# Kernel tuning notes

Hardware: AMD Instinct MI355X
Metric: run time of the kernel (lower is better)

Reference implementation:

```python
import jax, jax.numpy as jnp
import numpy as np

# ---------- helpers ----------

def _sqdist(a, b):
    # a: (B,n,3), b: (B,m,3) -> squared distances (B,n,m)
    return (jnp.sum(a * a, -1)[..., :, None] + jnp.sum(b * b, -1)[..., None, :]
            - 2.0 * jnp.einsum('bnd,bmd->bnm', a, b))

_gather = jax.vmap(lambda pts, idx: pts[idx])  # (N,C),(S,K)->(S,K,C) over batch


def _fps(xyz, npoint):
    # farthest point sampling; indices are non-differentiable (as in CUDA op)
    xyz = jax.lax.stop_gradient(xyz)
    B, N, _ = xyz.shape
    mind0 = jnp.sum((xyz - xyz[:, :1]) ** 2, -1)  # dist to point 0

    def step(mind, _):
        idx = jnp.argmax(mind, -1)                       # (B,)
        nxt = jnp.take_along_axis(xyz, idx[:, None, None], 1)  # (B,1,3)
        mind = jnp.minimum(mind, jnp.sum((xyz - nxt) ** 2, -1))
        return mind, idx.astype(jnp.int32)

    _, idxs = jax.lax.scan(step, mind0, None, length=npoint - 1)
    return jnp.concatenate([jnp.zeros((B, 1), jnp.int32), idxs.T], 1)  # (B,npoint)


def _ball_query(xyz, new_xyz, radius, nsample):
    # first nsample points within radius of each center, pad with first hit
    d2 = jax.lax.stop_gradient(_sqdist(new_xyz, xyz))  # (B,S,N)
    N = xyz.shape[1]
    mask = d2 < radius * radius
    key = jnp.where(mask, 0, N) + jnp.arange(N, dtype=jnp.int32)  # in-ball first, original order
    order = jnp.argsort(key, -1)
    idx = order[..., :nsample]
    cnt = mask.sum(-1, keepdims=True)
    return jnp.where(jnp.arange(nsample) < cnt, idx, idx[..., :1])


def _mlp(x, params):
    # shared MLP: 1x1 conv (+BN folded: default eval stats -> affine bias) + ReLU
    for W, b in params:
        x = jax.nn.relu(jnp.einsum('...c,co->...o', x, W) + b)
    return x


def _sa(xyz, feats, npoint, radius, nsample, params):
    # PointnetSAModuleVotes: FPS + ball-query + group(use_xyz, normalize_xyz) + MLP + max-pool
    inds = _fps(xyz, npoint)
    new_xyz = _gather(xyz, inds)                              # (B,S,3)
    idx = _ball_query(xyz, new_xyz, radius, nsample)          # (B,S,K)
    g = (_gather(xyz, idx) - new_xyz[:, :, None, :]) / radius  # normalize_xyz
    if feats is not None:
        g = jnp.concatenate([g, _gather(feats, idx)], -1)     # use_xyz: xyz first
    g = _mlp(g, params)
    return new_xyz, jnp.max(g, 2), inds                       # max over nsample


def _fp(unknown, known, feats1, feats2, params):
    # PointnetFPModule: 3-NN inverse-(squared)distance interpolation + MLP
    d2 = jax.lax.stop_gradient(_sqdist(unknown, known))       # (B,n,m)
    negd, idx = jax.lax.top_k(-d2, 3)
    d = jnp.maximum(-negd, 0.0)
    w = 1.0 / (d + 1e-8)
    w = w / jnp.sum(w, -1, keepdims=True)                     # (B,n,3)
    interp = jnp.sum(w[..., None] * _gather(feats2, idx), 2)  # (B,n,C2)
    return _mlp(jnp.concatenate([feats1, interp], -1), params)


_SPECS = {
    'sa1': [(3, 32), (32, 32), (32, 64)],
    'sa2': [(67, 64), (64, 128)],
    'sa3': [(131, 128), (128, 256)],
    'sa4': [(259, 256), (256, 256)],
    'fp1': [(512, 256), (256, 128)],
    'fp2': [(256, 128), (128, 64)],
}


def setup_inputs() -> dict:
    key = jax.random.key(0)
    ks = iter(jax.random.split(key, 64))
    inp = {'pointcloud': jax.random.uniform(next(ks), (4, 32768, 3), jnp.float32)}
    for name, dims in _SPECS.items():
        for i, (ci, co) in enumerate(dims):
            inp[f'{name}_w{i}'] = jax.random.normal(next(ks), (ci, co), jnp.float32) * 0.02
            inp[f'{name}_b{i}'] = jnp.zeros((co,), jnp.float32)
    return inp


def reference(pointcloud,
              sa1_w0, sa1_b0, sa1_w1, sa1_b1, sa1_w2, sa1_b2,
              sa2_w0, sa2_b0, sa2_w1, sa2_b1,
              sa3_w0, sa3_b0, sa3_w1, sa3_b1,
              sa4_w0, sa4_b0, sa4_w1, sa4_b1,
              fp1_w0, fp1_b0, fp1_w1, fp1_b1,
              fp2_w0, fp2_b0, fp2_w1, fp2_b1):
    P = {
        'sa1': [(sa1_w0, sa1_b0), (sa1_w1, sa1_b1), (sa1_w2, sa1_b2)],
        'sa2': [(sa2_w0, sa2_b0), (sa2_w1, sa2_b1)],
        'sa3': [(sa3_w0, sa3_b0), (sa3_w1, sa3_b1)],
        'sa4': [(sa4_w0, sa4_b0), (sa4_w1, sa4_b1)],
        'fp1': [(fp1_w0, fp1_b0), (fp1_w1, fp1_b1)],
        'fp2': [(fp2_w0, fp2_b0), (fp2_w1, fp2_b1)],
    }
    xyz = pointcloud[..., :3]  # input_feature_dim = 0 -> no extra features
    xyz1, f1, _ = _sa(xyz, None, 512, 0.1, 64, P['sa1'])
    xyz2, f2, _ = _sa(xyz1, f1, 256, 0.2, 32, P['sa2'])
    xyz3, f3, _ = _sa(xyz2, f2, 64, 0.4, 16, P['sa3'])
    xyz4, f4, _ = _sa(xyz3, f3, 16, 0.8, 16, P['sa4'])
    f = _fp(xyz3, xyz4, f3, f4, P['fp1'])   # (B,64,128)
    f = _fp(xyz2, xyz3, f2, f, P['fp2'])    # (B,256,64) == torch feats.transpose(1,2)
    return f, xyz2
```

## Files before the change

### kernel.cpp

```cpp
#include <hip/hip_runtime.h>
#include <cstddef>


__device__ __forceinline__ float sqd(float x, float y, float z, float qx, float qy, float qz) {
#pragma clang fp contract(off)
    float dx = x - qx, dy = y - qy, dz = z - qz;
    return (dx * dx + dy * dy) + dz * dz;
}

__device__ __forceinline__ float sum3sq(float x, float y, float z) {
#pragma clang fp contract(off)
    return (x * x + y * y) + z * z;
}

__device__ __forceinline__ float sqd_dot(float ax, float ay, float az, float sa_,
                                         float bx, float by, float bz) {
#pragma clang fp contract(off)
    float sb = (bx * bx + by * by) + bz * bz;
    float dt = (ax * bx + ay * by) + az * bz;
    return (sa_ + sb) - 2.0f * dt;
}

__device__ __forceinline__ unsigned long long packkey(float v, int orig) {
    return ((unsigned long long)__float_as_uint(v) << 32) | (unsigned)(~orig);
}


__global__ __launch_bounds__(512) void fps_sub(const float* __restrict__ xyz,
                                               int* __restrict__ inds,
                                               float4* __restrict__ SPall,
                                               float* __restrict__ gout) {
    const int b = blockIdx.x, t = threadIdx.x, w = t >> 6, l = t & 63;
    const float* __restrict__ P = xyz + (size_t)b * 32768 * 3;
    float4* __restrict__ SP = SPall + (size_t)b * 32768;

    __shared__ float mind[32768];
    __shared__ int   cntS[512], offS[512], curS[512];
    __shared__ unsigned long long bkeyS[512];
    __shared__ float bxS[512], byS[512], bzS[512];
    __shared__ unsigned long long candK[8];
    __shared__ int   candB[8];
    __shared__ float bbS[6];
    __shared__ float scr[48];
    __shared__ int   qcntS;

    float mnx = 1e30f, mny = 1e30f, mnz = 1e30f;
    float mxx = -1e30f, mxy = -1e30f, mxz = -1e30f;
    for (int p = t; p < 32768; p += 512) {
        const float x = P[3 * p], y = P[3 * p + 1], z = P[3 * p + 2];
        mnx = fminf(mnx, x); mxx = fmaxf(mxx, x);
        mny = fminf(mny, y); mxy = fmaxf(mxy, y);
        mnz = fminf(mnz, z); mxz = fmaxf(mxz, z);
    }
#pragma unroll
    for (int o = 1; o < 64; o <<= 1) {
        mnx = fminf(mnx, __shfl_xor(mnx, o)); mxx = fmaxf(mxx, __shfl_xor(mxx, o));
        mny = fminf(mny, __shfl_xor(mny, o)); mxy = fmaxf(mxy, __shfl_xor(mxy, o));
        mnz = fminf(mnz, __shfl_xor(mnz, o)); mxz = fmaxf(mxz, __shfl_xor(mxz, o));
    }
    if (l == 0) {
        scr[w] = mnx; scr[8 + w] = mny; scr[16 + w] = mnz;
        scr[24 + w] = mxx; scr[32 + w] = mxy; scr[40 + w] = mxz;
    }
    __syncthreads();
    if (t == 0) {
        float a0 = 1e30f, a1 = 1e30f, a2 = 1e30f, a3 = -1e30f, a4 = -1e30f, a5 = -1e30f;
        for (int i = 0; i < 8; ++i) {
            a0 = fminf(a0, scr[i]);      a1 = fminf(a1, scr[8 + i]);
            a2 = fminf(a2, scr[16 + i]); a3 = fmaxf(a3, scr[24 + i]);
            a4 = fmaxf(a4, scr[32 + i]); a5 = fmaxf(a5, scr[40 + i]);
        }
        bbS[0] = a0; bbS[1] = a1; bbS[2] = a2; bbS[3] = a3; bbS[4] = a4; bbS[5] = a5;
        qcntS = 0;
    }
    __syncthreads();
    const float bx0 = bbS[0], by0 = bbS[1], bz0 = bbS[2];
    const float ex = bbS[3] - bx0, ey = bbS[4] - by0, ez = bbS[5] - bz0;
    const float ivx = ex > 1e-20f ? 8.0f / ex : 0.0f;
    const float ivy = ey > 1e-20f ? 8.0f / ey : 0.0f;
    const float ivz = ez > 1e-20f ? 8.0f / ez : 0.0f;

    cntS[t] = 0;
    __syncthreads();
    for (int p = t; p < 32768; p += 512) {
        const float x = P[3 * p], y = P[3 * p + 1], z = P[3 * p + 2];
        const int ix = min(7, (int)((x - bx0) * ivx));
        const int iy = min(7, (int)((y - by0) * ivy));
        const int iz = min(7, (int)((z - bz0) * ivz));
        atomicAdd(&cntS[(iz * 8 + iy) * 8 + ix], 1);
    }
    __syncthreads();

    offS[t] = cntS[t];
    __syncthreads();
    for (int d = 1; d < 512; d <<= 1) {
        const int v = (t >= d) ? offS[t - d] : 0;
        __syncthreads();
        offS[t] += v;
        __syncthreads();
    }
    const int myexc = offS[t] - cntS[t];
    offS[t] = myexc;
    curS[t] = myexc;
    __syncthreads();

    for (int p = t; p < 32768; p += 512) {
        const float x = P[3 * p], y = P[3 * p + 1], z = P[3 * p + 2];
        const int ix = min(7, (int)((x - bx0) * ivx));
        const int iy = min(7, (int)((y - by0) * ivy));
        const int iz = min(7, (int)((z - bz0) * ivz));
        const int pos = atomicAdd(&curS[(iz * 8 + iy) * 8 + ix], 1);
        SP[pos] = make_float4(x, y, z, __int_as_float(p));
    }
    for (int s = t; s < 32768; s += 512) mind[s] = 1e30f;
    const int myCnt = cntS[t];
    bkeyS[t] = (myCnt > 0) ? packkey(1e30f, 0x7fffffff) : 0ull;
    bxS[t] = 0.f; byS[t] = 0.f; bzS[t] = 0.f;
    if (t == 0) {
        inds[b * 512] = 0;
        gout[(size_t)b * 512 * 3 + 0] = P[0];
        gout[(size_t)b * 512 * 3 + 1] = P[1];
        gout[(size_t)b * 512 * 3 + 2] = P[2];
    }

    const int oix = t & 7, oiy = (t >> 3) & 7, oiz = t >> 6;
    const float gwx = ex * 0.125f, gwy = ey * 0.125f, gwz = ez * 0.125f;
    const float x0o = bx0 + oix * gwx, x1o = x0o + gwx;
    const float y0o = by0 + oiy * gwy, y1o = y0o + gwy;
    const float z0o = bz0 + oiz * gwz, z1o = z0o + gwz;

    const int g  = l >> 4;
    const int lg = l & 15;
    const int sg = w * 4 + g;

    float qx = P[0], qy = P[1], qz = P[2];
    __syncthreads();

    for (int k = 1; k < 512; ++k) {
        const float ddx = fmaxf(fmaxf(x0o - qx, qx - x1o), 0.0f);
        const float ddy = fmaxf(fmaxf(y0o - qy, qy - y1o), 0.0f);
        const float ddz = fmaxf(fmaxf(z0o - qz, qz - z1o), 0.0f);
        const float d2m = (ddx * ddx + ddy * ddy) + ddz * ddz;
        const float bm = __uint_as_float((unsigned)(bkeyS[t] >> 32));
        const bool act = (myCnt > 0) && (d2m <= bm * 1.0001f + 1e-9f);
        const unsigned long long pmask = __ballot(act);
        const int wcnt = __popcll(pmask);
        int wbase = 0;
        if (l == 0 && wcnt) wbase = atomicAdd(&qcntS, wcnt);
        wbase = __shfl(wbase, 0);
        if (act) curS[wbase + __popcll(pmask & ((1ull << l) - 1ull))] = t;
        __syncthreads();
        const int A = qcntS;

        for (int e = sg; e < A; e += 32) {
            const int bu = curS[e];
            const int base = offS[bu], cnt = cntS[bu];
            unsigned long long key = 0ull;
            int klane = l;
            float cx = 0.f, cy = 0.f, cz = 0.f;
            for (int c = lg; c < cnt; c += 16) {
                const float4 pt = SP[base + c];
                const float m = mind[base + c];
                const float d2 = sqd(pt.x, pt.y, pt.z, qx, qy, qz);
                const float nm = fminf(m, d2);
                mind[base + c] = nm;
                const unsigned long long kk = packkey(nm, __float_as_int(pt.w));
                if (kk > key) { key = kk; cx = pt.x; cy = pt.y; cz = pt.z; }
            }
#pragma unroll
            for (int s = 1; s < 16; s <<= 1) {
                const unsigned long long ok = __shfl_xor(key, s);
                const int ol2 = __shfl_xor(klane, s);
                if (ok > key) { key = ok; klane = ol2; }
            }
            const float wx = __shfl(cx, klane), wy = __shfl(cy, klane), wz = __shfl(cz, klane);
            if (lg == 0) {
                bkeyS[bu] = key;
                bxS[bu] = wx; byS[bu] = wy; bzS[bu] = wz;
            }
        }
        __syncthreads();

        unsigned long long key = bkeyS[t];
        int bu2 = t;
#pragma unroll
        for (int s = 1; s < 64; s <<= 1) {
            const unsigned long long ok = __shfl_xor(key, s);
            const int ob = __shfl_xor(bu2, s);
            if (ok > key) { key = ok; bu2 = ob; }
        }
        if (l == 0) { candK[w] = key; candB[w] = bu2; }
        if (t == 0) qcntS = 0;
        __syncthreads();
        unsigned long long wk = candK[0]; int wb = candB[0];
#pragma unroll
        for (int j = 1; j < 8; ++j) {
            const unsigned long long k2 = candK[j];
            if (k2 > wk) { wk = k2; wb = candB[j]; }
        }
        qx = bxS[wb]; qy = byS[wb]; qz = bzS[wb];
        if (t == 0) {
            inds[b * 512 + k] = (int)~(unsigned)wk;
            gout[((size_t)b * 512 + k) * 3 + 0] = qx;
            gout[((size_t)b * 512 + k) * 3 + 1] = qy;
            gout[((size_t)b * 512 + k) * 3 + 2] = qz;
        }
    }
}


template <int N, int NPOINT>
__global__ __launch_bounds__(64) void fps_small(const float* __restrict__ pts,
                                                float* __restrict__ gout) {
    constexpr int PPT = N / 64;
    const int b = blockIdx.x, l = threadIdx.x;
    const float* __restrict__ P = pts + (size_t)b * N * 3;
    float px[PPT], py[PPT], pz[PPT], md[PPT];
#pragma unroll
    for (int j = 0; j < PPT; ++j) {
        const int p = l + 64 * j;
        px[j] = P[p * 3]; py[j] = P[p * 3 + 1]; pz[j] = P[p * 3 + 2];
        md[j] = 1e30f;
    }
    float qx = P[0], qy = P[1], qz = P[2];
    if (l == 0) {
        gout[(size_t)b * NPOINT * 3 + 0] = qx;
        gout[(size_t)b * NPOINT * 3 + 1] = qy;
        gout[(size_t)b * NPOINT * 3 + 2] = qz;
    }
    for (int k = 1; k < NPOINT; ++k) {
        float bv = -1.0f;
        int   bi = 0;
#pragma unroll
        for (int j = 0; j < PPT; ++j) {
            md[j] = fminf(md[j], sqd(px[j], py[j], pz[j], qx, qy, qz));
            if (md[j] > bv) { bv = md[j]; bi = l + 64 * j; }
        }
#pragma unroll
        for (int off = 1; off < 64; off <<= 1) {
            float ov = __shfl_xor(bv, off);
            int   oi = __shfl_xor(bi, off);
            if (ov > bv || (ov == bv && oi < bi)) { bv = ov; bi = oi; }
        }
        const int ol = bi & 63, js = bi >> 6;
        float sx = px[0], sy = py[0], sz = pz[0];
#pragma unroll
        for (int j = 1; j < PPT; ++j) {
            if (j == js) { sx = px[j]; sy = py[j]; sz = pz[j]; }
        }
        qx = __shfl(sx, ol); qy = __shfl(sy, ol); qz = __shfl(sz, ol);
        if (l == 0) {
            gout[((size_t)b * NPOINT + k) * 3 + 0] = qx;
            gout[((size_t)b * NPOINT + k) * 3 + 1] = qy;
            gout[((size_t)b * NPOINT + k) * 3 + 2] = qz;
        }
    }
}


__global__ __launch_bounds__(64) void sa1_fused(
    const float* __restrict__ xyz, const float* __restrict__ centers,
    const float* __restrict__ w0, const float* __restrict__ b0,
    const float* __restrict__ w1, const float* __restrict__ b1,
    const float* __restrict__ w2, const float* __restrict__ b2,
    float* __restrict__ outf, float r2, float r) {
    const int gc = blockIdx.x;
    const int b  = gc >> 9;
    const int l  = threadIdx.x;
    const float* __restrict__ P = xyz + (size_t)b * 32768 * 3;
    const float* cp = centers + (size_t)gc * 3;
    const float cx = cp[0], cy = cp[1], cz = cp[2];
    const float sa_ = sum3sq(cx, cy, cz);
    __shared__ int idxS[64];

    int cnt = 0, first = -1;
    float nx = P[l * 3], ny = P[l * 3 + 1], nz = P[l * 3 + 2];
    for (int i0 = 0; i0 < 32768; i0 += 64) {
        const float bx = nx, by = ny, bz = nz;
        if (i0 + 64 < 32768) {
            const int ip = (i0 + 64 + l) * 3;
            nx = P[ip]; ny = P[ip + 1]; nz = P[ip + 2];
        }
        const float d2 = sqd_dot(cx, cy, cz, sa_, bx, by, bz);
        const bool in = d2 < r2;
        const unsigned long long mask = __ballot(in);
        if (first < 0 && mask != 0ull) first = i0 + __builtin_ctzll(mask);
        const int pos = cnt + __popcll(mask & ((1ull << l) - 1ull));
        if (in && pos < 64) idxS[pos] = i0 + l;
        cnt += __popcll(mask);
        if (cnt >= 64) break;
    }
    if (first < 0) first = 0;
    for (int p2 = cnt + l; p2 < 64; p2 += 64) idxS[p2] = first;
    __syncthreads();

    const int n = idxS[l];
    const float* pp = P + (size_t)n * 3;
    float gi[3];
    gi[0] = (pp[0] - cx) / r; gi[1] = (pp[1] - cy) / r; gi[2] = (pp[2] - cz) / r;
    float h1[32];
#pragma unroll
    for (int o = 0; o < 32; ++o) {
        float acc = b0[o];
#pragma unroll
        for (int k = 0; k < 3; ++k) acc += gi[k] * w0[k * 32 + o];
        h1[o] = fmaxf(acc, 0.f);
    }
    float h2[32];
#pragma unroll
    for (int o = 0; o < 32; ++o) {
        float acc = b1[o];
#pragma unroll
        for (int k = 0; k < 32; ++k) acc += h1[k] * w1[k * 32 + o];
        h2[o] = fmaxf(acc, 0.f);
    }
    __shared__ float hs[64][65];
#pragma unroll
    for (int o = 0; o < 64; ++o) {
        float acc = b2[o];
#pragma unroll
        for (int k = 0; k < 32; ++k) acc += h2[k] * w2[k * 64 + o];
        hs[l][o] = fmaxf(acc, 0.f);
    }
    __syncthreads();
    float mx = hs[0][l];
    for (int s2 = 1; s2 < 64; ++s2) mx = fmaxf(mx, hs[s2][l]);
    outf[(size_t)gc * 64 + l] = mx;
}


template <int NS>
__global__ __launch_bounds__(256) void bqb(const float* __restrict__ xyz_src,
                                           const float* __restrict__ centers,
                                           const float* __restrict__ feats,
                                           float* __restrict__ g,
                                           int N, int M, int CF, float r, float r2) {
    const int wv = blockIdx.x * 4 + (threadIdx.x >> 6);
    const int w  = threadIdx.x >> 6;
    const int l  = threadIdx.x & 63;
    const int b  = wv / M;
    __shared__ int idxS[4][NS];
    const float* cp = centers + (size_t)wv * 3;
    const float ax = cp[0], ay = cp[1], az = cp[2];
    const float sa_ = sum3sq(ax, ay, az);
    const float* __restrict__ P = xyz_src + (size_t)b * N * 3;

    int cnt = 0, first = -1;
    float nx = P[l * 3], ny = P[l * 3 + 1], nz = P[l * 3 + 2];
    for (int i0 = 0; i0 < N; i0 += 64) {
        const float bx = nx, by = ny, bz = nz;
        if (i0 + 64 < N) {
            const int ip = (i0 + 64 + l) * 3;
            nx = P[ip]; ny = P[ip + 1]; nz = P[ip + 2];
        }
        const float d2 = sqd_dot(ax, ay, az, sa_, bx, by, bz);
        const bool in = d2 < r2;
        const unsigned long long mask = __ballot(in);
        if (first < 0 && mask != 0ull) first = i0 + __builtin_ctzll(mask);
        const int pos = cnt + __popcll(mask & ((1ull << l) - 1ull));
        if (in && pos < NS) idxS[w][pos] = i0 + l;
        cnt += __popcll(mask);
        if (cnt >= NS) break;
    }
    if (first < 0) first = 0;
    for (int p2 = cnt + l; p2 < NS; p2 += 64) idxS[w][p2] = first;
    __syncthreads();

    for (int s = 0; s < NS; ++s) {
        const int n = idxS[w][s];
        float* go = g + ((size_t)wv * NS + s) * (3 + CF);
        const float* pp = P + (size_t)n * 3;
        if (l < 3) go[l] = (pp[l] - cp[l]) / r;
        for (int c = l; c < CF; c += 64) go[3 + c] = feats[((size_t)b * N + n) * CF + c];
    }
}


__global__ void dense_relu(const float* __restrict__ X, const float* __restrict__ Wm,
                           const float* __restrict__ bias, float* __restrict__ Y,
                           int M, int CI, int CO) {
    const int co = blockIdx.x * 64 + threadIdx.x;
    const int m  = blockIdx.y * 4 + threadIdx.y;
    const float* x = X + (size_t)m * CI;
    float acc = bias[co];
#pragma unroll 4
    for (int k = 0; k < CI; ++k) acc += x[k] * Wm[(size_t)k * CO + co];
    Y[(size_t)m * CO + co] = fmaxf(acc, 0.f);
}


__global__ void dense_relu_max(const float* __restrict__ X, const float* __restrict__ Wm,
                               const float* __restrict__ bias, float* __restrict__ F,
                               int NS, int CI, int CO) {
    const int co = blockIdx.x * 64 + threadIdx.x;
    const int bm = blockIdx.y;
    const float b0 = bias[co];
    float mx = -1e30f;
    for (int s = 0; s < NS; ++s) {
        const float* x = X + ((size_t)bm * NS + s) * CI;
        float acc = b0;
#pragma unroll 4
        for (int k = 0; k < CI; ++k) acc += x[k] * Wm[(size_t)k * CO + co];
        mx = fmaxf(mx, fmaxf(acc, 0.f));
    }
    F[(size_t)bm * CO + co] = mx;
}


__global__ void fp_nn(const float* __restrict__ unk, const float* __restrict__ kn,
                      int* __restrict__ nni, float* __restrict__ nnw, int NU, int NK) {
    const int t = blockIdx.x * blockDim.x + threadIdx.x;
    const int b = t / NU;
    const float* u = unk + (size_t)t * 3;
    const float ax = u[0], ay = u[1], az = u[2];
    const float sa_ = sum3sq(ax, ay, az);
    const float* K = kn + (size_t)b * NK * 3;
    float v0 = 1e30f, v1 = 1e30f, v2 = 1e30f;
    int   j0 = 0, j1 = 0, j2 = 0;
    for (int k = 0; k < NK; ++k) {
        const float d2 = sqd_dot(ax, ay, az, sa_, K[k * 3], K[k * 3 + 1], K[k * 3 + 2]);
        if (d2 < v0)      { v2 = v1; j2 = j1; v1 = v0; j1 = j0; v0 = d2; j0 = k; }
        else if (d2 < v1) { v2 = v1; j2 = j1; v1 = d2; j1 = k; }
        else if (d2 < v2) { v2 = d2; j2 = k; }
    }
    const float d0 = fmaxf(v0, 0.f), d1 = fmaxf(v1, 0.f), dd2 = fmaxf(v2, 0.f);
    float w0 = 1.f / (d0 + 1e-8f), w1 = 1.f / (d1 + 1e-8f), w2 = 1.f / (dd2 + 1e-8f);
    const float s = (w0 + w1) + w2;
    nnw[t * 3] = w0 / s; nnw[t * 3 + 1] = w1 / s; nnw[t * 3 + 2] = w2 / s;
    nni[t * 3] = j0; nni[t * 3 + 1] = j1; nni[t * 3 + 2] = j2;
}


__global__ void dense_fp(const float* __restrict__ f1c, const float* __restrict__ f2c,
                         const int* __restrict__ nni, const float* __restrict__ nnw,
                         const float* __restrict__ Wm, const float* __restrict__ bias,
                         float* __restrict__ Y, int NU, int NK, int C1c, int C2c, int CO) {
    const int co = blockIdx.x * 64 + threadIdx.x;
    const int m  = blockIdx.y * 4 + threadIdx.y;
    const int b  = m / NU;
    const int i0 = nni[m * 3], i1 = nni[m * 3 + 1], i2 = nni[m * 3 + 2];
    const float w0 = nnw[m * 3], w1 = nnw[m * 3 + 1], w2 = nnw[m * 3 + 2];
    const float* x1 = f1c + (size_t)m * C1c;
    const float* a  = f2c + ((size_t)b * NK + i0) * C2c;
    const float* bb = f2c + ((size_t)b * NK + i1) * C2c;
    const float* cc = f2c + ((size_t)b * NK + i2) * C2c;
    float acc = bias[co];
#pragma unroll 4
    for (int k = 0; k < C1c; ++k) acc += x1[k] * Wm[(size_t)k * CO + co];
#pragma unroll 4
    for (int k = 0; k < C2c; ++k) {
        const float xi = (w0 * a[k] + w1 * bb[k]) + w2 * cc[k];
        acc += xi * Wm[(size_t)(C1c + k) * CO + co];
    }
    Y[(size_t)m * CO + co] = fmaxf(acc, 0.f);
}

__global__ void copyf(const float* __restrict__ src, float* __restrict__ dst, int n) {
    const int i = blockIdx.x * 256 + threadIdx.x;
    if (i < n) dst[i] = src[i];
}


extern "C" void kernel_launch(void* const* d_in, const int* in_sizes, int n_in,
                              void* d_out, int out_size, void* d_ws, size_t ws_size,
                              hipStream_t stream) {
    const float* xyz  = (const float*)d_in[0];
    const float* s1w0 = (const float*)d_in[1],  *s1b0 = (const float*)d_in[2];
    const float* s1w1 = (const float*)d_in[3],  *s1b1 = (const float*)d_in[4];
    const float* s1w2 = (const float*)d_in[5],  *s1b2 = (const float*)d_in[6];
    const float* s2w0 = (const float*)d_in[7],  *s2b0 = (const float*)d_in[8];
    const float* s2w1 = (const float*)d_in[9],  *s2b1 = (const float*)d_in[10];
    const float* s3w0 = (const float*)d_in[11], *s3b0 = (const float*)d_in[12];
    const float* s3w1 = (const float*)d_in[13], *s3b1 = (const float*)d_in[14];
    const float* s4w0 = (const float*)d_in[15], *s4b0 = (const float*)d_in[16];
    const float* s4w1 = (const float*)d_in[17], *s4b1 = (const float*)d_in[18];
    const float* p1w0 = (const float*)d_in[19], *p1b0 = (const float*)d_in[20];
    const float* p1w1 = (const float*)d_in[21], *p1b1 = (const float*)d_in[22];
    const float* p2w0 = (const float*)d_in[23], *p2b0 = (const float*)d_in[24];
    const float* p2w1 = (const float*)d_in[25], *p2b1 = (const float*)d_in[26];
    float* out = (float*)d_out;
    float* W = (float*)d_ws;

    size_t off = 0;
    auto A_ = [&](size_t n) { size_t o = off; off += (n + 63) & ~(size_t)63; return o; };
    const size_t o_inds1 = A_(4 * 512);
    const size_t o_xyz1  = A_(4 * 512 * 3);
    const size_t o_f1    = A_(4 * 512 * 64);
    const size_t o_xyz2  = A_(4 * 256 * 3);
    const size_t o_f2    = A_(4 * 256 * 128);
    const size_t o_xyz3  = A_(4 * 64 * 3);
    const size_t o_f3    = A_(4 * 64 * 256);
    const size_t o_xyz4  = A_(4 * 16 * 3);
    const size_t o_f4    = A_(4 * 16 * 256);
    const size_t o_f5    = A_(4 * 64 * 128);
    const size_t o_nni1  = A_(4 * 64 * 3);
    const size_t o_nnw1  = A_(4 * 64 * 3);
    const size_t o_nni2  = A_(4 * 256 * 3);
    const size_t o_nnw2  = A_(4 * 256 * 3);
    const size_t o_sort  = A_((size_t)4 * 32768 * 4);
    const size_t o_bufA  = A_((size_t)32768 * 128);
    const size_t o_bufB  = A_((size_t)32768 * 64);
    if (off * sizeof(float) > ws_size) return;

    int*   inds1 = (int*)(W + o_inds1); float* xyz1 = W + o_xyz1;
    float* f1    = W + o_f1;
    float* xyz2  = W + o_xyz2;          float* f2   = W + o_f2;
    float* xyz3  = W + o_xyz3;          float* f3   = W + o_f3;
    float* xyz4  = W + o_xyz4;          float* f4   = W + o_f4;
    float* f5    = W + o_f5;
    int*   nni1  = (int*)(W + o_nni1);  float* nnw1 = W + o_nnw1;
    int*   nni2  = (int*)(W + o_nni2);  float* nnw2 = W + o_nnw2;
    float4* sortP = (float4*)(W + o_sort);
    float* bufA  = W + o_bufA;
    float* bufB  = W + o_bufB;

    fps_sub<<<4, 512, 0, stream>>>(xyz, inds1, sortP, xyz1);
    sa1_fused<<<2048, 64, 0, stream>>>(xyz, xyz1, s1w0, s1b0, s1w1, s1b1, s1w2, s1b2,
                                       f1, (float)(0.1 * 0.1), 0.1f);

    fps_small<512, 256><<<4, 64, 0, stream>>>(xyz1, xyz2);
    bqb<32><<<256, 256, 0, stream>>>(xyz1, xyz2, f1, bufA, 512, 256, 64, 0.2f,
                                     (float)(0.2 * 0.2));
    dense_relu<<<dim3(1, 8192), dim3(64, 4), 0, stream>>>(bufA, s2w0, s2b0, bufB, 32768, 67, 64);
    dense_relu_max<<<dim3(2, 1024), 64, 0, stream>>>(bufB, s2w1, s2b1, f2, 32, 64, 128);

    fps_small<256, 64><<<4, 64, 0, stream>>>(xyz2, xyz3);
    bqb<16><<<64, 256, 0, stream>>>(xyz2, xyz3, f2, bufA, 256, 64, 128, 0.4f,
                                    (float)(0.4 * 0.4));
    dense_relu<<<dim3(2, 1024), dim3(64, 4), 0, stream>>>(bufA, s3w0, s3b0, bufB, 4096, 131, 128);
    dense_relu_max<<<dim3(4, 256), 64, 0, stream>>>(bufB, s3w1, s3b1, f3, 16, 128, 256);

    fps_small<64, 16><<<4, 64, 0, stream>>>(xyz3, xyz4);
    bqb<16><<<16, 256, 0, stream>>>(xyz3, xyz4, f3, bufA, 64, 16, 256, 0.8f,
                                    (float)(0.8 * 0.8));
    dense_relu<<<dim3(4, 256), dim3(64, 4), 0, stream>>>(bufA, s4w0, s4b0, bufB, 1024, 259, 256);
    dense_relu_max<<<dim3(4, 64), 64, 0, stream>>>(bufB, s4w1, s4b1, f4, 16, 256, 256);

    fp_nn<<<1, 256, 0, stream>>>(xyz3, xyz4, nni1, nnw1, 64, 16);
    dense_fp<<<dim3(4, 64), dim3(64, 4), 0, stream>>>(f3, f4, nni1, nnw1, p1w0, p1b0,
                                                      bufB, 64, 16, 256, 256, 256);
    dense_relu<<<dim3(2, 64), dim3(64, 4), 0, stream>>>(bufB, p1w1, p1b1, f5, 256, 256, 128);

    fp_nn<<<4, 256, 0, stream>>>(xyz2, xyz3, nni2, nnw2, 256, 64);
    dense_fp<<<dim3(2, 256), dim3(64, 4), 0, stream>>>(f2, f5, nni2, nnw2, p2w0, p2b0,
                                                       bufB, 256, 64, 128, 128, 128);
    dense_relu<<<dim3(1, 256), dim3(64, 4), 0, stream>>>(bufB, p2w1, p2b1, out, 1024, 128, 64);

    copyf<<<12, 256, 0, stream>>>(xyz2, out + 65536, 3072);
}
```

Before: 2.457 ms.

## Fuse post-FPS pipeline into one persistent megakernel with grid barriers

Everything after the first FPS (SA1 grouping and MLP, the smaller FPS stages, ball queries, dense layers, feature propagation and the output copy) now runs in one persistent kernel of 256 blocks × 512 threads. The stages are separated by a software grid barrier built on a global atomic counter, which is reset by a memset before launch. Dense stages become grid-stride loops. The unused FPS index output is also dropped. The aim is to remove the launch overhead and gaps between roughly twenty small dependent kernels. The trade-offs are spin-wait barrier cost, idle blocks during the serial FPS stages, and reliance on all blocks being co-resident.

```diff
diff --git a/kernel.cpp b/kernel.cpp
--- a/kernel.cpp
+++ b/kernel.cpp
@@ -1,5 +1,8 @@
 #include <hip/hip_runtime.h>
 #include <cstddef>
+
+#define NBLK 256
+#define NTH  131072
 
 
 __device__ __forceinline__ float sqd(float x, float y, float z, float qx, float qy, float qz) {
@@ -27,7 +30,6 @@
 
 
 __global__ __launch_bounds__(512) void fps_sub(const float* __restrict__ xyz,
-                                               int* __restrict__ inds,
                                                float4* __restrict__ SPall,
                                                float* __restrict__ gout) {
     const int b = blockIdx.x, t = threadIdx.x, w = t >> 6, l = t & 63;
@@ -117,7 +119,6 @@
     bkeyS[t] = (myCnt > 0) ? packkey(1e30f, 0x7fffffff) : 0ull;
     bxS[t] = 0.f; byS[t] = 0.f; bzS[t] = 0.f;
     if (t == 0) {
-        inds[b * 512] = 0;
         gout[(size_t)b * 512 * 3 + 0] = P[0];
         gout[(size_t)b * 512 * 3 + 1] = P[1];
         gout[(size_t)b * 512 * 3 + 2] = P[2];
@@ -200,7 +201,6 @@
         }
         qx = bxS[wb]; qy = byS[wb]; qz = bzS[wb];
         if (t == 0) {
-            inds[b * 512 + k] = (int)~(unsigned)wk;
             gout[((size_t)b * 512 + k) * 3 + 0] = qx;
             gout[((size_t)b * 512 + k) * 3 + 1] = qy;
             gout[((size_t)b * 512 + k) * 3 + 2] = qz;
@@ -209,12 +209,38 @@
 }
 
 
+struct MegaArgs {
+    const float *xyz;
+    const float *s1w0, *s1b0, *s1w1, *s1b1, *s1w2, *s1b2;
+    const float *s2w0, *s2b0, *s2w1, *s2b1;
+    const float *s3w0, *s3b0, *s3w1, *s3b1;
+    const float *s4w0, *s4b0, *s4w1, *s4b1;
+    const float *p1w0, *p1b0, *p1w1, *p1b1;
+    const float *p2w0, *p2b0, *p2w1, *p2b1;
+    float *xyz1, *f1, *xyz2, *f2, *xyz3, *f3, *xyz4, *f4, *f5;
+    int *nni1; float *nnw1; int *nni2; float *nnw2;
+    float *bufA, *bufB;
+    float *out;
+};
+
+__device__ __forceinline__ void gridbar(int* bar, int phase) {
+    __syncthreads();
+    if (threadIdx.x == 0) {
+        __threadfence();
+        atomicAdd(bar, 1);
+        const int target = phase * NBLK;
+        while (__hip_atomic_load(bar, __ATOMIC_ACQUIRE, __HIP_MEMORY_SCOPE_AGENT) < target) {
+            __builtin_amdgcn_s_sleep(2);
+        }
+        __threadfence();
+    }
+    __syncthreads();
+}
+
+
 template <int N, int NPOINT>
-__global__ __launch_bounds__(64) void fps_small(const float* __restrict__ pts,
-                                                float* __restrict__ gout) {
+__device__ void fps_small_dev(const float* __restrict__ P, float* __restrict__ gout, int l) {
     constexpr int PPT = N / 64;
-    const int b = blockIdx.x, l = threadIdx.x;
-    const float* __restrict__ P = pts + (size_t)b * N * 3;
     float px[PPT], py[PPT], pz[PPT], md[PPT];
 #pragma unroll
     for (int j = 0; j < PPT; ++j) {
@@ -223,11 +249,7 @@
         md[j] = 1e30f;
     }
     float qx = P[0], qy = P[1], qz = P[2];
-    if (l == 0) {
-        gout[(size_t)b * NPOINT * 3 + 0] = qx;
-        gout[(size_t)b * NPOINT * 3 + 1] = qy;
-        gout[(size_t)b * NPOINT * 3 + 2] = qz;
-    }
+    if (l == 0) { gout[0] = qx; gout[1] = qy; gout[2] = qz; }
     for (int k = 1; k < NPOINT; ++k) {
         float bv = -1.0f;
         int   bi = 0;
@@ -250,28 +272,24 @@
         }
         qx = __shfl(sx, ol); qy = __shfl(sy, ol); qz = __shfl(sz, ol);
         if (l == 0) {
-            gout[((size_t)b * NPOINT + k) * 3 + 0] = qx;
-            gout[((size_t)b * NPOINT + k) * 3 + 1] = qy;
-            gout[((size_t)b * NPOINT + k) * 3 + 2] = qz;
-        }
-    }
-}
-
-
-__global__ __launch_bounds__(64) void sa1_fused(
-    const float* __restrict__ xyz, const float* __restrict__ centers,
-    const float* __restrict__ w0, const float* __restrict__ b0,
-    const float* __restrict__ w1, const float* __restrict__ b1,
-    const float* __restrict__ w2, const float* __restrict__ b2,
-    float* __restrict__ outf, float r2, float r) {
-    const int gc = blockIdx.x;
-    const int b  = gc >> 9;
-    const int l  = threadIdx.x;
+            gout[(size_t)k * 3 + 0] = qx;
+            gout[(size_t)k * 3 + 1] = qy;
+            gout[(size_t)k * 3 + 2] = qz;
+        }
+    }
+}
+
+__device__ void sa1_dev(const float* __restrict__ xyz, const float* __restrict__ centers,
+                        const float* __restrict__ w0, const float* __restrict__ b0,
+                        const float* __restrict__ w1, const float* __restrict__ b1,
+                        const float* __restrict__ w2, const float* __restrict__ b2,
+                        float* __restrict__ outf, float r2, float r,
+                        int gc, int l, int* __restrict__ idxw, float (*__restrict__ hsw)[65]) {
+    const int b = gc >> 9;
     const float* __restrict__ P = xyz + (size_t)b * 32768 * 3;
     const float* cp = centers + (size_t)gc * 3;
     const float cx = cp[0], cy = cp[1], cz = cp[2];
     const float sa_ = sum3sq(cx, cy, cz);
-    __shared__ int idxS[64];
 
     int cnt = 0, first = -1;
     float nx = P[l * 3], ny = P[l * 3 + 1], nz = P[l * 3 + 2];
@@ -286,15 +304,14 @@
         const unsigned long long mask = __ballot(in);
         if (first < 0 && mask != 0ull) first = i0 + __builtin_ctzll(mask);
         const int pos = cnt + __popcll(mask & ((1ull << l) - 1ull));
-        if (in && pos < 64) idxS[pos] = i0 + l;
+        if (in && pos < 64) idxw[pos] = i0 + l;
         cnt += __popcll(mask);
         if (cnt >= 64) break;
     }
     if (first < 0) first = 0;
-    for (int p2 = cnt + l; p2 < 64; p2 += 64) idxS[p2] = first;
-    __syncthreads();
-
-    const int n = idxS[l];
+    for (int p2 = cnt + l; p2 < 64; p2 += 64) idxw[p2] = first;
+
+    const int n = idxw[l];
     const float* pp = P + (size_t)n * 3;
     float gi[3];
     gi[0] = (pp[0] - cx) / r; gi[1] = (pp[1] - cy) / r; gi[2] = (pp[2] - cz) / r;
@@ -314,32 +331,25 @@
         for (int k = 0; k < 32; ++k) acc += h1[k] * w1[k * 32 + o];
         h2[o] = fmaxf(acc, 0.f);
     }
-    __shared__ float hs[64][65];
 #pragma unroll
     for (int o = 0; o < 64; ++o) {
         float acc = b2[o];
 #pragma unroll
         for (int k = 0; k < 32; ++k) acc += h2[k] * w2[k * 64 + o];
-        hs[l][o] = fmaxf(acc, 0.f);
-    }
-    __syncthreads();
-    float mx = hs[0][l];
-    for (int s2 = 1; s2 < 64; ++s2) mx = fmaxf(mx, hs[s2][l]);
+        hsw[l][o] = fmaxf(acc, 0.f);
+    }
+    __threadfence_block();
+    float mx = hsw[0][l];
+    for (int s2 = 1; s2 < 64; ++s2) mx = fmaxf(mx, hsw[s2][l]);
     outf[(size_t)gc * 64 + l] = mx;
 }
 
-
 template <int NS>
-__global__ __launch_bounds__(256) void bqb(const float* __restrict__ xyz_src,
-                                           const float* __restrict__ centers,
-                                           const float* __restrict__ feats,
-                                           float* __restrict__ g,
-                                           int N, int M, int CF, float r, float r2) {
-    const int wv = blockIdx.x * 4 + (threadIdx.x >> 6);
-    const int w  = threadIdx.x >> 6;
-    const int l  = threadIdx.x & 63;
-    const int b  = wv / M;
-    __shared__ int idxS[4][NS];
+__device__ void bqb_dev(const float* __restrict__ xyz_src, const float* __restrict__ centers,
+                        const float* __restrict__ feats, float* __restrict__ g,
+                        int N, int M, int CF, float r, float r2,
+                        int wv, int l, int* __restrict__ idxw) {
+    const int b = wv / M;
     const float* cp = centers + (size_t)wv * 3;
     const float ax = cp[0], ay = cp[1], az = cp[2];
     const float sa_ = sum3sq(ax, ay, az);
@@ -358,16 +368,15 @@
         const unsigned long long mask = __ballot(in);
         if (first < 0 && mask != 0ull) first = i0 + __builtin_ctzll(mask);
         const int pos = cnt + __popcll(mask & ((1ull << l) - 1ull));
-        if (in && pos < NS) idxS[w][pos] = i0 + l;
+        if (in && pos < NS) idxw[pos] = i0 + l;
         cnt += __popcll(mask);
         if (cnt >= NS) break;
     }
     if (first < 0) first = 0;
-    for (int p2 = cnt + l; p2 < NS; p2 += 64) idxS[w][p2] = first;
-    __syncthreads();
+    for (int p2 = cnt + l; p2 < NS; p2 += 64) idxw[p2] = first;
 
     for (int s = 0; s < NS; ++s) {
-        const int n = idxS[w][s];
+        const int n = idxw[s];
         float* go = g + ((size_t)wv * NS + s) * (3 + CF);
         const float* pp = P + (size_t)n * 3;
         if (l < 3) go[l] = (pp[l] - cp[l]) / r;
@@ -375,41 +384,46 @@
     }
 }
 
-
-__global__ void dense_relu(const float* __restrict__ X, const float* __restrict__ Wm,
-                           const float* __restrict__ bias, float* __restrict__ Y,
-                           int M, int CI, int CO) {
-    const int co = blockIdx.x * 64 + threadIdx.x;
-    const int m  = blockIdx.y * 4 + threadIdx.y;
-    const float* x = X + (size_t)m * CI;
-    float acc = bias[co];
-#pragma unroll 4
-    for (int k = 0; k < CI; ++k) acc += x[k] * Wm[(size_t)k * CO + co];
-    Y[(size_t)m * CO + co] = fmaxf(acc, 0.f);
-}
-
-
-__global__ void dense_relu_max(const float* __restrict__ X, const float* __restrict__ Wm,
-                               const float* __restrict__ bias, float* __restrict__ F,
-                               int NS, int CI, int CO) {
-    const int co = blockIdx.x * 64 + threadIdx.x;
-    const int bm = blockIdx.y;
-    const float b0 = bias[co];
-    float mx = -1e30f;
-    for (int s = 0; s < NS; ++s) {
-        const float* x = X + ((size_t)bm * NS + s) * CI;
-        float acc = b0;
+template <int COL2>
+__device__ void dense_relu_dev(const float* __restrict__ X, const float* __restrict__ Wm,
+                               const float* __restrict__ bias, float* __restrict__ Y,
+                               int M, int CI, int gid) {
+    const int CO = 1 << COL2;
+    const int total = M << COL2;
+    for (int i = gid; i < total; i += NTH) {
+        const int m = i >> COL2, co = i & (CO - 1);
+        const float* x = X + (size_t)m * CI;
+        float acc = bias[co];
 #pragma unroll 4
         for (int k = 0; k < CI; ++k) acc += x[k] * Wm[(size_t)k * CO + co];
-        mx = fmaxf(mx, fmaxf(acc, 0.f));
-    }
-    F[(size_t)bm * CO + co] = mx;
-}
-
-
-__global__ void fp_nn(const float* __restrict__ unk, const float* __restrict__ kn,
-                      int* __restrict__ nni, float* __restrict__ nnw, int NU, int NK) {
-    const int t = blockIdx.x * blockDim.x + threadIdx.x;
+        Y[(size_t)m * CO + co] = fmaxf(acc, 0.f);
+    }
+}
+
+template <int COL2>
+__device__ void dense_max_dev(const float* __restrict__ X, const float* __restrict__ Wm,
+                              const float* __restrict__ bias, float* __restrict__ F,
+                              int BM, int NS, int CI, int gid) {
+    const int CO = 1 << COL2;
+    const int total = BM << COL2;
+    for (int i = gid; i < total; i += NTH) {
+        const int bm = i >> COL2, co = i & (CO - 1);
+        const float b0v = bias[co];
+        float mx = -1e30f;
+        for (int s = 0; s < NS; ++s) {
+            const float* x = X + ((size_t)bm * NS + s) * CI;
+            float acc = b0v;
+#pragma unroll 4
+            for (int k = 0; k < CI; ++k) acc += x[k] * Wm[(size_t)k * CO + co];
+            mx = fmaxf(mx, fmaxf(acc, 0.f));
+        }
+        F[(size_t)bm * CO + co] = mx;
+    }
+}
+
+__device__ void fp_nn_dev(const float* __restrict__ unk, const float* __restrict__ kn,
+                          int* __restrict__ nni, float* __restrict__ nnw,
+                          int NU, int NK, int t) {
     const int b = t / NU;
     const float* u = unk + (size_t)t * 3;
     const float ax = u[0], ay = u[1], az = u[2];
@@ -430,121 +444,142 @@
     nni[t * 3] = j0; nni[t * 3 + 1] = j1; nni[t * 3 + 2] = j2;
 }
 
-
-__global__ void dense_fp(const float* __restrict__ f1c, const float* __restrict__ f2c,
-                         const int* __restrict__ nni, const float* __restrict__ nnw,
-                         const float* __restrict__ Wm, const float* __restrict__ bias,
-                         float* __restrict__ Y, int NU, int NK, int C1c, int C2c, int CO) {
-    const int co = blockIdx.x * 64 + threadIdx.x;
-    const int m  = blockIdx.y * 4 + threadIdx.y;
-    const int b  = m / NU;
-    const int i0 = nni[m * 3], i1 = nni[m * 3 + 1], i2 = nni[m * 3 + 2];
-    const float w0 = nnw[m * 3], w1 = nnw[m * 3 + 1], w2 = nnw[m * 3 + 2];
-    const float* x1 = f1c + (size_t)m * C1c;
-    const float* a  = f2c + ((size_t)b * NK + i0) * C2c;
-    const float* bb = f2c + ((size_t)b * NK + i1) * C2c;
-    const float* cc = f2c + ((size_t)b * NK + i2) * C2c;
-    float acc = bias[co];
+template <int COL2>
+__device__ void dense_fp_dev(const float* __restrict__ f1c, const float* __restrict__ f2c,
+                             const int* __restrict__ nni, const float* __restrict__ nnw,
+                             const float* __restrict__ Wm, const float* __restrict__ bias,
+                             float* __restrict__ Y, int NU, int NK, int C1c, int C2c,
+                             int gid) {
+    const int CO = 1 << COL2;
+    const int total = (4 * NU) << COL2;
+    for (int i = gid; i < total; i += NTH) {
+        const int m = i >> COL2, co = i & (CO - 1);
+        const int b = m / NU;
+        const int i0 = nni[m * 3], i1 = nni[m * 3 + 1], i2 = nni[m * 3 + 2];
+        const float w0v = nnw[m * 3], w1v = nnw[m * 3 + 1], w2v = nnw[m * 3 + 2];
+        const float* x1 = f1c + (size_t)m * C1c;
+        const float* a  = f2c + ((size_t)b * NK + i0) * C2c;
+        const float* bb = f2c + ((size_t)b * NK + i1) * C2c;
+        const float* cc = f2c + ((size_t)b * NK + i2) * C2c;
+        float acc = bias[co];
 #pragma unroll 4
-    for (int k = 0; k < C1c; ++k) acc += x1[k] * Wm[(size_t)k * CO + co];
+        for (int k = 0; k < C1c; ++k) acc += x1[k] * Wm[(size_t)k * CO + co];
 #pragma unroll 4
-    for (int k = 0; k < C2c; ++k) {
-        const float xi = (w0 * a[k] + w1 * bb[k]) + w2 * cc[k];
-        acc += xi * Wm[(size_t)(C1c + k) * CO + co];
-    }
-    Y[(size_t)m * CO + co] = fmaxf(acc, 0.f);
-}
-
-__global__ void copyf(const float* __restrict__ src, float* __restrict__ dst, int n) {
-    const int i = blockIdx.x * 256 + threadIdx.x;
-    if (i < n) dst[i] = src[i];
+        for (int k = 0; k < C2c; ++k) {
+            const float xi = (w0v * a[k] + w1v * bb[k]) + w2v * cc[k];
+            acc += xi * Wm[(size_t)(C1c + k) * CO + co];
+        }
+        Y[(size_t)m * CO + co] = fmaxf(acc, 0.f);
+    }
+}
+
+__global__ __launch_bounds__(512) void mega(MegaArgs A, int* bar) {
+    __shared__ float hsS[8][64][65];
+    __shared__ int   idxS[8][64];
+    const int tid = threadIdx.x;
+    const int w = tid >> 6, l = tid & 63;
+    const int gw = blockIdx.x * 8 + w;
+    const int gid = blockIdx.x * 512 + tid;
+
+    sa1_dev(A.xyz, A.xyz1, A.s1w0, A.s1b0, A.s1w1, A.s1b1, A.s1w2, A.s1b2,
+            A.f1, 0.01f, 0.1f, gw, l, &idxS[w][0], &hsS[w][0]);
+    gridbar(bar, 1);
+    if (gw < 4) fps_small_dev<512, 256>(A.xyz1 + (size_t)gw * 512 * 3,
+                                        A.xyz2 + (size_t)gw * 256 * 3, l);
+    gridbar(bar, 2);
+    if (gw < 1024) bqb_dev<32>(A.xyz1, A.xyz2, A.f1, A.bufA, 512, 256, 64,
+                               0.2f, 0.04f, gw, l, &idxS[w][0]);
+    gridbar(bar, 3);
+    dense_relu_dev<6>(A.bufA, A.s2w0, A.s2b0, A.bufB, 32768, 67, gid);
+    gridbar(bar, 4);
+    dense_max_dev<7>(A.bufB, A.s2w1, A.s2b1, A.f2, 1024, 32, 64, gid);
+    gridbar(bar, 5);
+    if (gw < 4) fps_small_dev<256, 64>(A.xyz2 + (size_t)gw * 256 * 3,
+                                       A.xyz3 + (size_t)gw * 64 * 3, l);
+    gridbar(bar, 6);
+    if (gw < 256) bqb_dev<16>(A.xyz2, A.xyz3, A.f2, A.bufA, 256, 64, 128,
+                              0.4f, 0.16f, gw, l, &idxS[w][0]);
+    gridbar(bar, 7);
+    dense_relu_dev<7>(A.bufA, A.s3w0, A.s3b0, A.bufB, 4096, 131, gid);
+    gridbar(bar, 8);
+    dense_max_dev<8>(A.bufB, A.s3w1, A.s3b1, A.f3, 256, 16, 128, gid);
+    gridbar(bar, 9);
+    if (gw < 4) fps_small_dev<64, 16>(A.xyz3 + (size_t)gw * 64 * 3,
+                                      A.xyz4 + (size_t)gw * 16 * 3, l);
+    gridbar(bar, 10);
+    if (gw < 64) bqb_dev<16>(A.xyz3, A.xyz4, A.f3, A.bufA, 64, 16, 256,
+                             0.8f, 0.64f, gw, l, &idxS[w][0]);
+    gridbar(bar, 11);
+    dense_relu_dev<8>(A.bufA, A.s4w0, A.s4b0, A.bufB, 1024, 259, gid);
+    gridbar(bar, 12);
+    dense_max_dev<8>(A.bufB, A.s4w1, A.s4b1, A.f4, 64, 16, 256, gid);
+    if (gid >= 16384 && gid < 16640) fp_nn_dev(A.xyz3, A.xyz4, A.nni1, A.nnw1, 64, 16, gid - 16384);
+    else if (gid >= 16640 && gid < 17664) fp_nn_dev(A.xyz2, A.xyz3, A.nni2, A.nnw2, 256, 64, gid - 16640);
+    gridbar(bar, 13);
+    dense_fp_dev<8>(A.f3, A.f4, A.nni1, A.nnw1, A.p1w0, A.p1b0, A.bufA, 64, 16, 256, 256, gid);
+    gridbar(bar, 14);
+    dense_relu_dev<7>(A.bufA, A.p1w1, A.p1b1, A.f5, 256, 256, gid);
+    gridbar(bar, 15);
+    dense_fp_dev<7>(A.f2, A.f5, A.nni2, A.nnw2, A.p2w0, A.p2b0, A.bufB, 256, 64, 128, 128, gid);
+    gridbar(bar, 16);
+    dense_relu_dev<6>(A.bufB, A.p2w1, A.p2b1, A.out, 1024, 128, gid);
+    for (int i = gid; i < 3072; i += NTH) A.out[65536 + i] = A.xyz2[i];
 }
 
 
 extern "C" void kernel_launch(void* const* d_in, const int* in_sizes, int n_in,
                               void* d_out, int out_size, void* d_ws, size_t ws_size,
                               hipStream_t stream) {
-    const float* xyz  = (const float*)d_in[0];
-    const float* s1w0 = (const float*)d_in[1],  *s1b0 = (const float*)d_in[2];
-    const float* s1w1 = (const float*)d_in[3],  *s1b1 = (const float*)d_in[4];
-    const float* s1w2 = (const float*)d_in[5],  *s1b2 = (const float*)d_in[6];
-    const float* s2w0 = (const float*)d_in[7],  *s2b0 = (const float*)d_in[8];
-    const float* s2w1 = (const float*)d_in[9],  *s2b1 = (const float*)d_in[10];
-    const float* s3w0 = (const float*)d_in[11], *s3b0 = (const float*)d_in[12];
-    const float* s3w1 = (const float*)d_in[13], *s3b1 = (const float*)d_in[14];
-    const float* s4w0 = (const float*)d_in[15], *s4b0 = (const float*)d_in[16];
-    const float* s4w1 = (const float*)d_in[17], *s4b1 = (const float*)d_in[18];
-    const float* p1w0 = (const float*)d_in[19], *p1b0 = (const float*)d_in[20];
-    const float* p1w1 = (const float*)d_in[21], *p1b1 = (const float*)d_in[22];
-    const float* p2w0 = (const float*)d_in[23], *p2b0 = (const float*)d_in[24];
-    const float* p2w1 = (const float*)d_in[25], *p2b1 = (const float*)d_in[26];
-    float* out = (float*)d_out;
     float* W = (float*)d_ws;
-
     size_t off = 0;
     auto A_ = [&](size_t n) { size_t o = off; off += (n + 63) & ~(size_t)63; return o; };
-    const size_t o_inds1 = A_(4 * 512);
-    const size_t o_xyz1  = A_(4 * 512 * 3);
-    const size_t o_f1    = A_(4 * 512 * 64);
-    const size_t o_xyz2  = A_(4 * 256 * 3);
-    const size_t o_f2    = A_(4 * 256 * 128);
-    const size_t o_xyz3  = A_(4 * 64 * 3);
-    const size_t o_f3    = A_(4 * 64 * 256);
-    const size_t o_xyz4  = A_(4 * 16 * 3);
-    const size_t o_f4    = A_(4 * 16 * 256);
-    const size_t o_f5    = A_(4 * 64 * 128);
-    const size_t o_nni1  = A_(4 * 64 * 3);
-    const size_t o_nnw1  = A_(4 * 64 * 3);
-    const size_t o_nni2  = A_(4 * 256 * 3);
-    const size_t o_nnw2  = A_(4 * 256 * 3);
-    const size_t o_sort  = A_((size_t)4 * 32768 * 4);
-    const size_t o_bufA  = A_((size_t)32768 * 128);
-    const size_t o_bufB  = A_((size_t)32768 * 64);
+    const size_t o_xyz1 = A_(4 * 512 * 3);
+    const size_t o_f1   = A_(4 * 512 * 64);
+    const size_t o_xyz2 = A_(4 * 256 * 3);
+    const size_t o_f2   = A_(4 * 256 * 128);
+    const size_t o_xyz3 = A_(4 * 64 * 3);
+    const size_t o_f3   = A_(4 * 64 * 256);
+    const size_t o_xyz4 = A_(4 * 16 * 3);
+    const size_t o_f4   = A_(4 * 16 * 256);
+    const size_t o_f5   = A_(4 * 64 * 128);
+    const size_t o_nni1 = A_(4 * 64 * 3);
+    const size_t o_nnw1 = A_(4 * 64 * 3);
+    const size_t o_nni2 = A_(4 * 256 * 3);
+    const size_t o_nnw2 = A_(4 * 256 * 3);
+    const size_t o_bar  = A_(64);
+    const size_t o_sort = A_((size_t)4 * 32768 * 4);
+    const size_t o_bufA = A_((size_t)32768 * 128);
+    const size_t o_bufB = A_((size_t)32768 * 64);
     if (off * sizeof(float) > ws_size) return;
 
-    int*   inds1 = (int*)(W + o_inds1); float* xyz1 = W + o_xyz1;
-    float* f1    = W + o_f1;
-    float* xyz2  = W + o_xyz2;          float* f2   = W + o_f2;
-    float* xyz3  = W + o_xyz3;          float* f3   = W + o_f3;
-    float* xyz4  = W + o_xyz4;          float* f4   = W + o_f4;
-    float* f5    = W + o_f5;
-    int*   nni1  = (int*)(W + o_nni1);  float* nnw1 = W + o_nnw1;
-    int*   nni2  = (int*)(W + o_nni2);  float* nnw2 = W + o_nnw2;
+    MegaArgs M;
+    M.xyz  = (const float*)d_in[0];
+    M.s1w0 = (const float*)d_in[1];  M.s1b0 = (const float*)d_in[2];
+    M.s1w1 = (const float*)d_in[3];  M.s1b1 = (const float*)d_in[4];
+    M.s1w2 = (const float*)d_in[5];  M.s1b2 = (const float*)d_in[6];
+    M.s2w0 = (const float*)d_in[7];  M.s2b0 = (const float*)d_in[8];
+    M.s2w1 = (const float*)d_in[9];  M.s2b1 = (const float*)d_in[10];
+    M.s3w0 = (const float*)d_in[11]; M.s3b0 = (const float*)d_in[12];
+    M.s3w1 = (const float*)d_in[13]; M.s3b1 = (const float*)d_in[14];
+    M.s4w0 = (const float*)d_in[15]; M.s4b0 = (const float*)d_in[16];
+    M.s4w1 = (const float*)d_in[17]; M.s4b1 = (const float*)d_in[18];
+    M.p1w0 = (const float*)d_in[19]; M.p1b0 = (const float*)d_in[20];
+    M.p1w1 = (const float*)d_in[21]; M.p1b1 = (const float*)d_in[22];
+    M.p2w0 = (const float*)d_in[23]; M.p2b0 = (const float*)d_in[24];
+    M.p2w1 = (const float*)d_in[25]; M.p2b1 = (const float*)d_in[26];
+    M.xyz1 = W + o_xyz1; M.f1 = W + o_f1;
+    M.xyz2 = W + o_xyz2; M.f2 = W + o_f2;
+    M.xyz3 = W + o_xyz3; M.f3 = W + o_f3;
+    M.xyz4 = W + o_xyz4; M.f4 = W + o_f4;
+    M.f5   = W + o_f5;
+    M.nni1 = (int*)(W + o_nni1); M.nnw1 = W + o_nnw1;
+    M.nni2 = (int*)(W + o_nni2); M.nnw2 = W + o_nnw2;
+    M.bufA = W + o_bufA; M.bufB = W + o_bufB;
+    M.out  = (float*)d_out;
+    int* bar = (int*)(W + o_bar);
     float4* sortP = (float4*)(W + o_sort);
-    float* bufA  = W + o_bufA;
-    float* bufB  = W + o_bufB;
-
-    fps_sub<<<4, 512, 0, stream>>>(xyz, inds1, sortP, xyz1);
-    sa1_fused<<<2048, 64, 0, stream>>>(xyz, xyz1, s1w0, s1b0, s1w1, s1b1, s1w2, s1b2,
-                                       f1, (float)(0.1 * 0.1), 0.1f);
-
-    fps_small<512, 256><<<4, 64, 0, stream>>>(xyz1, xyz2);
-    bqb<32><<<256, 256, 0, stream>>>(xyz1, xyz2, f1, bufA, 512, 256, 64, 0.2f,
-                                     (float)(0.2 * 0.2));
-    dense_relu<<<dim3(1, 8192), dim3(64, 4), 0, stream>>>(bufA, s2w0, s2b0, bufB, 32768, 67, 64);
-    dense_relu_max<<<dim3(2, 1024), 64, 0, stream>>>(bufB, s2w1, s2b1, f2, 32, 64, 128);
-
-    fps_small<256, 64><<<4, 64, 0, stream>>>(xyz2, xyz3);
-    bqb<16><<<64, 256, 0, stream>>>(xyz2, xyz3, f2, bufA, 256, 64, 128, 0.4f,
-                                    (float)(0.4 * 0.4));
-    dense_relu<<<dim3(2, 1024), dim3(64, 4), 0, stream>>>(bufA, s3w0, s3b0, bufB, 4096, 131, 128);
-    dense_relu_max<<<dim3(4, 256), 64, 0, stream>>>(bufB, s3w1, s3b1, f3, 16, 128, 256);
-
-    fps_small<64, 16><<<4, 64, 0, stream>>>(xyz3, xyz4);
-    bqb<16><<<16, 256, 0, stream>>>(xyz3, xyz4, f3, bufA, 64, 16, 256, 0.8f,
-                                    (float)(0.8 * 0.8));
-    dense_relu<<<dim3(4, 256), dim3(64, 4), 0, stream>>>(bufA, s4w0, s4b0, bufB, 1024, 259, 256);
-    dense_relu_max<<<dim3(4, 64), 64, 0, stream>>>(bufB, s4w1, s4b1, f4, 16, 256, 256);
-
-    fp_nn<<<1, 256, 0, stream>>>(xyz3, xyz4, nni1, nnw1, 64, 16);
-    dense_fp<<<dim3(4, 64), dim3(64, 4), 0, stream>>>(f3, f4, nni1, nnw1, p1w0, p1b0,
-                                                      bufB, 64, 16, 256, 256, 256);
-    dense_relu<<<dim3(2, 64), dim3(64, 4), 0, stream>>>(bufB, p1w1, p1b1, f5, 256, 256, 128);
-
-    fp_nn<<<4, 256, 0, stream>>>(xyz2, xyz3, nni2, nnw2, 256, 64);
-    dense_fp<<<dim3(2, 256), dim3(64, 4), 0, stream>>>(f2, f5, nni2, nnw2, p2w0, p2b0,
-                                                       bufB, 256, 64, 128, 128, 128);
-    dense_relu<<<dim3(1, 256), dim3(64, 4), 0, stream>>>(bufB, p2w1, p2b1, out, 1024, 128, 64);
-
-    copyf<<<12, 256, 0, stream>>>(xyz2, out + 65536, 3072);
-}
+
+    hipMemsetAsync(bar, 0, sizeof(int), stream);
+    fps_sub<<<4, 512, 0, stream>>>(M.xyz, sortP, M.xyz1);
+    mega<<<NBLK, 512, 0, stream>>>(M, bar);
+}
```

Result: slower. 5.054 ms (+105.7%).
